# Kernel tuning notes

Hardware: AMD Instinct MI355X
Metric: run time of the kernel (lower is better)

Reference implementation:

```python
import jax, jax.numpy as jnp
import numpy as np

T, B = 128, 512
OBS_DIM = 512
HIDDEN = 512
ACTION_DIM = 18
LN_EPS = 1e-6  # flax LayerNorm default


def _layer_norm(x, scale, bias):
    m = jnp.mean(x, axis=-1, keepdims=True)
    v = jnp.var(x, axis=-1, keepdims=True)
    return (x - m) * jax.lax.rsqrt(v + LN_EPS) * scale + bias


def setup_inputs() -> dict:
    key = jax.random.key(0)
    ks = jax.random.split(key, 16)
    sc = lambda k, sh: jax.random.normal(k, sh, jnp.float32) * (1.0 / np.sqrt(sh[0]))
    d = {}
    d['hidden'] = jax.random.normal(ks[0], (B, HIDDEN), jnp.float32)
    d['obs'] = jax.random.normal(ks[1], (T, B, OBS_DIM), jnp.float32)
    d['dones'] = jax.random.randint(ks[2], (T, B), 0, 2).astype(bool)
    d['last_acts'] = jax.random.randint(ks[3], (T, B), 0, ACTION_DIM, dtype=jnp.int32)
    in0 = OBS_DIM + ACTION_DIM
    d['w0'] = sc(ks[4], (in0, HIDDEN)); d['b0'] = jnp.zeros((HIDDEN,), jnp.float32)
    d['ln0_s'] = jnp.ones((HIDDEN,), jnp.float32); d['ln0_b'] = jnp.zeros((HIDDEN,), jnp.float32)
    d['w1'] = sc(ks[5], (HIDDEN, HIDDEN)); d['b1'] = jnp.zeros((HIDDEN,), jnp.float32)
    d['ln1_s'] = jnp.ones((HIDDEN,), jnp.float32); d['ln1_b'] = jnp.zeros((HIDDEN,), jnp.float32)
    d['w_ir'] = sc(ks[6], (HIDDEN, HIDDEN)); d['b_ir'] = jnp.zeros((HIDDEN,), jnp.float32)
    d['w_iz'] = sc(ks[7], (HIDDEN, HIDDEN)); d['b_iz'] = jnp.zeros((HIDDEN,), jnp.float32)
    d['w_in'] = sc(ks[8], (HIDDEN, HIDDEN)); d['b_in'] = jnp.zeros((HIDDEN,), jnp.float32)
    d['w_hr'] = sc(ks[9], (HIDDEN, HIDDEN))
    d['w_hz'] = sc(ks[10], (HIDDEN, HIDDEN))
    d['w_hn'] = sc(ks[11], (HIDDEN, HIDDEN)); d['b_hn'] = jnp.zeros((HIDDEN,), jnp.float32)
    d['w_out'] = sc(ks[12], (HIDDEN, ACTION_DIM)); d['b_out'] = jnp.zeros((ACTION_DIM,), jnp.float32)
    return d


def reference(hidden, obs, dones, last_acts,
              w0, b0, ln0_s, ln0_b, w1, b1, ln1_s, ln1_b,
              w_ir, b_ir, w_iz, b_iz, w_in, b_in,
              w_hr, w_hz, w_hn, b_hn, w_out, b_out):
    # embed last actions and concat with obs: [T, B, obs_dim + action_dim]
    one_hot = jax.nn.one_hot(last_acts, ACTION_DIM, dtype=obs.dtype)
    x = jnp.concatenate([obs, one_hot], axis=-1)
    # MLP encoder: Dense -> LayerNorm -> relu, applied over all (T, B) at once
    x = jax.nn.relu(_layer_norm(x @ w0 + b0, ln0_s, ln0_b))
    x = jax.nn.relu(_layer_norm(x @ w1 + b1, ln1_s, ln1_b))

    # ScannedRNN: GRUCell with reset-to-zero carry on done, scanned over time
    def step(h, xs):
        xt, dt = xs  # xt: [B, H], dt: [B] bool
        h = jnp.where(dt[:, None], jnp.zeros_like(h), h)
        r = jax.nn.sigmoid(xt @ w_ir + b_ir + h @ w_hr)
        z = jax.nn.sigmoid(xt @ w_iz + b_iz + h @ w_hz)
        n = jnp.tanh(xt @ w_in + b_in + r * (h @ w_hn + b_hn))
        h_new = (1.0 - z) * n + z * h
        return h_new, h_new

    new_hidden, y = jax.lax.scan(step, hidden, (x, dones))
    q_vals = y @ w_out + b_out  # [T, B, action_dim]
    return new_hidden, q_vals
```

## Files before the change

### kernel.cpp

```cpp
#include <hip/hip_runtime.h>
#include <cstdint>
#include <cstddef>


#define TT 128
#define BBATCH 512
#define HH 512
#define MM 65536
#define AD 18
#define GSTEPS 8
#define FSTRIDE 32
#define READY_U32 1064960

typedef __attribute__((ext_vector_type(8))) short short8;
typedef __attribute__((ext_vector_type(4))) float float4v;
typedef __attribute__((ext_vector_type(4))) unsigned int uint4v;

__device__ __forceinline__ unsigned short f2bf(float f) {
  union { float f; unsigned int u; } v; v.f = f;
  unsigned int r = v.u + 0x7fffu + ((v.u >> 16) & 1u);
  return (unsigned short)(r >> 16);
}
__device__ __forceinline__ float bf2f(unsigned short h) {
  union { unsigned int u; float f; } v; v.u = ((unsigned int)h) << 16;
  return v.f;
}

__device__ __forceinline__ unsigned int load_u32_coh(const unsigned int* p) {
  unsigned int v;
  asm volatile("global_load_dword %0, %1, off sc0 sc1\n\ts_waitcnt vmcnt(0)"
               : "=v"(v) : "v"(p) : "memory");
  return v;
}
__device__ __forceinline__ void store_u32_coh(unsigned int* p, unsigned int v) {
  asm volatile("global_store_dword %0, %1, off sc0 sc1"
               :: "v"(p), "v"(v) : "memory");
}
__device__ __forceinline__ void store_u64_coh(void* p, unsigned long long v) {
  asm volatile("global_store_dwordx2 %0, %1, off sc0 sc1"
               :: "v"(p), "v"(v) : "memory");
}

typedef __attribute__((address_space(3))) unsigned int* lds_u32p;
typedef const __attribute__((address_space(1))) unsigned int* glb_u32p;
__device__ __forceinline__ void async16(void* lds, const void* g) {
  __builtin_amdgcn_global_load_lds(
      (glb_u32p)(unsigned long long)g,
      (lds_u32p)(unsigned int)(unsigned long long)lds, 16, 0, 0);
}


__global__ __launch_bounds__(256) void k_conv_obs(
    const float* __restrict__ src, unsigned short* __restrict__ dst,
    unsigned int* __restrict__ flag) {
  if (blockIdx.x == 0 && threadIdx.x == 0) *flag = 0u;
  int i = blockIdx.x * 256 + threadIdx.x;
  float4v v = ((const float4v*)src)[i];
  unsigned long long pk = (unsigned long long)f2bf(v[0])
      | ((unsigned long long)f2bf(v[1]) << 16)
      | ((unsigned long long)f2bf(v[2]) << 32)
      | ((unsigned long long)f2bf(v[3]) << 48);
  ((unsigned long long*)dst)[i] = pk;
}

__global__ __launch_bounds__(256) void k_prep_t(
    const float* __restrict__ w0, const float* __restrict__ w1,
    const float* __restrict__ wir, const float* __restrict__ wiz,
    const float* __restrict__ win,
    unsigned short* __restrict__ W0at, unsigned short* __restrict__ W1t,
    unsigned short* __restrict__ Wit) {
  int o = blockIdx.x * 256 + threadIdx.x;
  int n = o >> 9, k = o & 511;
  int z = blockIdx.y;
  const float* s = (z == 0) ? w0 : (z == 1) ? w1 : (z == 2) ? wir
                 : (z == 3) ? wiz : win;
  unsigned short b = f2bf(s[k * 512 + n]);
  if (z == 0) W0at[o] = b;
  else if (z == 1) W1t[o] = b;
  else Wit[(size_t)(z - 2) * 262144 + o] = b;
}

__global__ __launch_bounds__(256) void k_prep_whf(
    const float* __restrict__ whr, const float* __restrict__ whz,
    const float* __restrict__ whn, unsigned short* __restrict__ Whf) {
  int i = blockIdx.x * 256 + threadIdx.x;
  int k = i / 1536, n = i - k * 1536;
  const float* s = (n < 512) ? whr : (n < 1024) ? whz : whn;
  float v = s[k * 512 + (n & 511)];
  Whf[((size_t)(k >> 3) * 1536 + n) * 8 + (k & 7)] = f2bf(v);
}

__global__ __launch_bounds__(256) void k_prep_misc(
    const float* __restrict__ w0, const float* __restrict__ bir,
    const float* __restrict__ biz, const float* __restrict__ bin,
    const float* __restrict__ wout, const float* __restrict__ hidden,
    const int* __restrict__ dI,
    unsigned short* __restrict__ w0act, float* __restrict__ gib,
    unsigned short* __restrict__ WoutT, unsigned short* __restrict__ hbuf,
    unsigned int* __restrict__ flag) {
  int i = blockIdx.x * 256 + threadIdx.x;
  if (i < 9216) {
    int a = i >> 9, n = i & 511;
    w0act[i] = f2bf(w0[(512 + a) * 512 + n]);
  }
  if (i < 1536)
    gib[i] = (i < 512) ? bir[i] : (i < 1024) ? biz[i - 512] : bin[i - 1024];
  if (i < 32768) {
    int n = i >> 9, k = i & 511;
    WoutT[i] = f2bf(n < AD ? wout[k * AD + n] : 0.f);
  }
  if (i < 262144) hbuf[i] = f2bf(hidden[i]);
  if (i < 16384) { if (dI[i] & 0xFFFFFFFE) atomicOr(flag, 1u); }
}

__global__ __launch_bounds__(256) void k_zero(unsigned int* __restrict__ p) {
  int i = (blockIdx.x * 256 + threadIdx.x) * 4;
  if (i < READY_U32) *(uint4v*)(p + i) = (uint4v){0u, 0u, 0u, 0u};
}


template <int MODE>
__global__ __launch_bounds__(512, 1) void k_enc(
    const unsigned short* __restrict__ Ab,
    const unsigned short* __restrict__ Btb,
    unsigned short* __restrict__ Cb,
    const float* __restrict__ bias,
    const float* __restrict__ lnS, const float* __restrict__ lnB,
    const unsigned short* __restrict__ gW,
    const int* __restrict__ acts) {
  __shared__ unsigned short As[8192];
  __shared__ unsigned short Bs[32768];
  __shared__ float part[128][4][2];
  __shared__ float stats[128][2];

  const int tid = threadIdx.x, wave = tid >> 6, lane = tid & 63;
  const int quad = lane >> 4, l15 = lane & 15;
  const int wm = wave >> 2, wn = wave & 3;
  const int m0 = blockIdx.x * 128;
  const int g = (MODE == 2) ? blockIdx.y : 0;
  const unsigned short* Bt = Btb + (size_t)g * 262144;
  const float* bi = bias + g * 512;

  float4v acc[4][8];
#pragma unroll
  for (int a = 0; a < 4; ++a)
#pragma unroll
    for (int b = 0; b < 8; ++b) acc[a][b] = (float4v){0.f, 0.f, 0.f, 0.f};

  for (int k0 = 0; k0 < 512; k0 += 64) {
#pragma unroll
    for (int r = 0; r < 2; ++r) {
      int u = r * 512 + tid;
      int ch = u >> 7, mm = u & 127;
      async16(&As[(size_t)(r * 512 + wave * 64) * 8],
              Ab + (size_t)(m0 + mm) * 512 + k0 + ch * 8);
    }
#pragma unroll
    for (int r = 0; r < 8; ++r) {
      int u = r * 512 + tid;
      int ch = u >> 9, nn = u & 511;
      async16(&Bs[(size_t)(r * 512 + wave * 64) * 8],
              Bt + (size_t)nn * 512 + k0 + ch * 8);
    }
    __syncthreads();
#pragma unroll
    for (int kk = 0; kk < 2; ++kk) {
      short8 afr[4], bfr[8];
#pragma unroll
      for (int mi = 0; mi < 4; ++mi)
        afr[mi] = *(const short8*)
            &As[((kk * 4 + quad) * 128 + wm * 64 + mi * 16 + l15) * 8];
#pragma unroll
      for (int ni = 0; ni < 8; ++ni)
        bfr[ni] = *(const short8*)
            &Bs[((kk * 4 + quad) * 512 + wn * 128 + ni * 16 + l15) * 8];
#pragma unroll
      for (int mi = 0; mi < 4; ++mi)
#pragma unroll
        for (int ni = 0; ni < 8; ++ni)
          acc[mi][ni] = __builtin_amdgcn_mfma_f32_16x16x32_bf16(
              afr[mi], bfr[ni], acc[mi][ni], 0, 0, 0);
    }
    __syncthreads();
  }

  float bcol[8];
#pragma unroll
  for (int ni = 0; ni < 8; ++ni) bcol[ni] = bi[wn * 128 + ni * 16 + l15];
#pragma unroll
  for (int mi = 0; mi < 4; ++mi)
#pragma unroll
    for (int i = 0; i < 4; ++i) {
      int row = m0 + wm * 64 + mi * 16 + quad * 4 + i;
      int arow = (MODE == 0) ? acts[row] : 0;
#pragma unroll
      for (int ni = 0; ni < 8; ++ni) {
        float v = acc[mi][ni][i] + bcol[ni];
        if (MODE == 0) v += bf2f(gW[arow * 512 + wn * 128 + ni * 16 + l15]);
        acc[mi][ni][i] = v;
      }
    }

  if (MODE <= 1) {
#pragma unroll
    for (int mi = 0; mi < 4; ++mi)
#pragma unroll
      for (int i = 0; i < 4; ++i) {
        float s = 0.f, q = 0.f;
#pragma unroll
        for (int ni = 0; ni < 8; ++ni) {
          float v = acc[mi][ni][i];
          s += v; q += v * v;
        }
#pragma unroll
        for (int d = 1; d < 16; d <<= 1) {
          s += __shfl_xor(s, d, 64);
          q += __shfl_xor(q, d, 64);
        }
        if (l15 == 0) {
          int rowl = wm * 64 + mi * 16 + quad * 4 + i;
          part[rowl][wn][0] = s;
          part[rowl][wn][1] = q;
        }
      }
    __syncthreads();
    if (tid < 128) {
      float s = part[tid][0][0] + part[tid][1][0] + part[tid][2][0] + part[tid][3][0];
      float q = part[tid][0][1] + part[tid][1][1] + part[tid][2][1] + part[tid][3][1];
      float mean = s * (1.f / 512.f);
      float var = fmaxf(q * (1.f / 512.f) - mean * mean, 0.f);
      stats[tid][0] = mean;
      stats[tid][1] = rsqrtf(var + 1e-6f);
    }
    __syncthreads();
    float sc8[8], cb8[8];
#pragma unroll
    for (int ni = 0; ni < 8; ++ni) {
      int col = wn * 128 + ni * 16 + l15;
      sc8[ni] = lnS[col];
      cb8[ni] = lnB[col];
    }
#pragma unroll
    for (int mi = 0; mi < 4; ++mi)
#pragma unroll
      for (int i = 0; i < 4; ++i) {
        int rowl = wm * 64 + mi * 16 + quad * 4 + i;
        float mean = stats[rowl][0], rstd = stats[rowl][1];
        int row = m0 + rowl;
#pragma unroll
        for (int ni = 0; ni < 8; ++ni) {
          int col = wn * 128 + ni * 16 + l15;
          float v = fmaxf((acc[mi][ni][i] - mean) * rstd * sc8[ni] + cb8[ni], 0.f);
          Cb[(size_t)row * 512 + col] = f2bf(v);
        }
      }
  } else {
#pragma unroll
    for (int mi = 0; mi < 4; ++mi)
#pragma unroll
      for (int i = 0; i < 4; ++i) {
        int row = m0 + wm * 64 + mi * 16 + quad * 4 + i;
        int t = row >> 9, b = row & 511;
#pragma unroll
        for (int ni = 0; ni < 8; ++ni) {
          int c = wn * 128 + ni * 16 + l15;
          size_t dst = ((size_t)((b >> 6) * 32 + (c >> 4)) * 128 + t) * 3072
                     + (size_t)g * 1024 + (b & 63) * 16 + (c & 15);
          Cb[dst] = f2bf(acc[mi][ni][i]);
        }
      }
  }
}


__global__ __launch_bounds__(256, 1) void k_gru(
    const unsigned short* __restrict__ Whf, const unsigned short* __restrict__ gin,
    const float* __restrict__ bhn, const int* __restrict__ dI,
    const unsigned char* __restrict__ dB, const unsigned int* __restrict__ flag,
    const unsigned short* __restrict__ hbuf, unsigned short* __restrict__ ybuf,
    float* __restrict__ outh, unsigned int* __restrict__ ready) {
  __shared__ __align__(16) unsigned short gin_lds[2][GSTEPS * 3 * 64 * 16];
  __shared__ unsigned char d_lds[TT * 64];

  const int tid = threadIdx.x, wave = tid >> 6, lane = tid & 63;
  const int quad = lane >> 4, l15 = lane & 15;
  const int rt = blockIdx.x & 7;
  const int cc = blockIdx.x >> 3;
  const int r0b = rt * 64;
  const int rowb = wave * 16 + l15;
  const int row = r0b + rowb;
  const int c0 = cc * 16 + quad * 4;
  const int bytemode = (int)(*flag);
  const float4v bhn4 = *(const float4v*)(bhn + c0);

  const unsigned short* gsrc = gin + (size_t)(rt * 32 + cc) * 128 * 3072;

  auto stage_gin = [&](int buf, int t0) {
    const unsigned short* src = gsrc + (size_t)t0 * 3072;
#pragma unroll
    for (int r = 0; r < 12; ++r) {
      async16(&gin_lds[buf][(size_t)(r * 256 + wave * 64) * 8],
              src + (size_t)(r * 256 + tid) * 8);
    }
  };

  stage_gin(0, 0);
#pragma unroll
  for (int r = 0; r < 32; ++r) {
    int idx = r * 256 + tid;
    int t = idx >> 6, rr = idx & 63;
    int gidx = t * 512 + r0b + rr;
    d_lds[idx] = bytemode ? dB[gidx] : (unsigned char)(dI[gidx] != 0);
  }

  short8 bw[3][16];
#pragma unroll
  for (int kc = 0; kc < 16; ++kc)
#pragma unroll
    for (int g = 0; g < 3; ++g) {
      size_t u = (size_t)(kc * 4 + quad) * 1536 + (g * 512 + cc * 16 + l15);
      bw[g][kc] = *(const short8*)(Whf + u * 8);
    }

  float hprev[4];
  {
    unsigned long long w = *(const unsigned long long*)(hbuf + (size_t)row * 512 + c0);
#pragma unroll
    for (int i = 0; i < 4; ++i) hprev[i] = bf2f((unsigned short)(w >> (16 * i)));
  }

  __syncthreads();

  for (int t = 0; t < TT; ++t) {
    if (t > 0) {
      if (wave == 0) {
        const unsigned int* fp =
            ready + (((size_t)rt * 130 + t) * 32 + (lane & 31)) * FSTRIDE;
        unsigned int v;
        int guard = 0;
        do {
          v = load_u32_coh(fp);
        } while (__ballot(v == 0u) != 0ull && ++guard < (1 << 22));
      }
      __syncthreads();
      asm volatile("" ::: "memory");
    }

    const unsigned short* hsrc =
        (t == 0) ? hbuf : ybuf + (size_t)(t - 1) * 262144;
    const unsigned short* ap = hsrc + (size_t)row * 512 + quad * 8;
    short8 af[16];
#pragma unroll
    for (int kc = 0; kc < 16; ++kc) af[kc] = *(const short8*)(ap + kc * 32);

    const int dd = (int)d_lds[(t << 6) + rowb];
    if (dd) {
      const short8 z8 = {0, 0, 0, 0, 0, 0, 0, 0};
#pragma unroll
      for (int kc = 0; kc < 16; ++kc) af[kc] = z8;
    }

    if ((t & (GSTEPS - 1)) == 0 && t + GSTEPS < TT)
      stage_gin(((t >> 3) + 1) & 1, t + GSTEPS);

    const int sl = t & (GSTEPS - 1), bufc = (t >> 3) & 1;
    float gr[4], gz[4], gn[4];
    {
      const unsigned short* gl =
          &gin_lds[bufc][((size_t)(sl * 3) * 64 + rowb) * 16 + quad * 4];
      unsigned long long w0 = *(const unsigned long long*)(gl);
      unsigned long long w1 = *(const unsigned long long*)(gl + 1024);
      unsigned long long w2 = *(const unsigned long long*)(gl + 2048);
#pragma unroll
      for (int i = 0; i < 4; ++i) {
        gr[i] = bf2f((unsigned short)(w0 >> (16 * i)));
        gz[i] = bf2f((unsigned short)(w1 >> (16 * i)));
        gn[i] = bf2f((unsigned short)(w2 >> (16 * i)));
      }
    }

    float4v a0 = {0.f, 0.f, 0.f, 0.f}, a1 = a0, a2 = a0;
#pragma unroll
    for (int kc = 0; kc < 16; ++kc) {
      a0 = __builtin_amdgcn_mfma_f32_16x16x32_bf16(bw[0][kc], af[kc], a0, 0, 0, 0);
      a1 = __builtin_amdgcn_mfma_f32_16x16x32_bf16(bw[1][kc], af[kc], a1, 0, 0, 0);
      a2 = __builtin_amdgcn_mfma_f32_16x16x32_bf16(bw[2][kc], af[kc], a2, 0, 0, 0);
    }

    unsigned short* ydst = ybuf + (size_t)t * 262144;
    float hv[4];
#pragma unroll
    for (int i = 0; i < 4; ++i) {
      float hold = dd ? 0.f : hprev[i];
      float r = 1.f / (1.f + __expf(-(a0[i] + gr[i])));
      float z = 1.f / (1.f + __expf(-(a1[i] + gz[i])));
      float npre = gn[i] + r * (a2[i] + bhn4[i]);
      float n = 1.f - 2.f / (1.f + __expf(2.f * npre));
      hv[i] = (1.f - z) * n + z * hold;
      hprev[i] = hv[i];
    }
    {
      unsigned long long pk = (unsigned long long)f2bf(hv[0])
          | ((unsigned long long)f2bf(hv[1]) << 16)
          | ((unsigned long long)f2bf(hv[2]) << 32)
          | ((unsigned long long)f2bf(hv[3]) << 48);
      store_u64_coh(ydst + (size_t)row * 512 + c0, pk);
    }
    if (t == TT - 1) {
      float4v o = {hv[0], hv[1], hv[2], hv[3]};
      *(float4v*)(outh + (size_t)row * 512 + c0) = o;
    }

    __syncthreads();
    if (tid == 0)
      store_u32_coh(&ready[(((size_t)rt * 130 + t + 1) * 32 + cc) * FSTRIDE], 1u);
  }
}


__global__ __launch_bounds__(256) void k_qout(
    const unsigned short* __restrict__ Yb, const unsigned short* __restrict__ Wt,
    const float* __restrict__ bout, float* __restrict__ Q) {
  __shared__ unsigned short As[8192];
  __shared__ unsigned short Bs[4096];
  const int tid = threadIdx.x, wave = tid >> 6, lane = tid & 63;
  const int quad = lane >> 4, l15 = lane & 15;
  const int m0 = blockIdx.x * 128;

  float4v acc[2][4];
#pragma unroll
  for (int a = 0; a < 2; ++a)
#pragma unroll
    for (int b = 0; b < 4; ++b) acc[a][b] = (float4v){0.f, 0.f, 0.f, 0.f};

  for (int k0 = 0; k0 < 512; k0 += 64) {
#pragma unroll
    for (int r = 0; r < 4; ++r) {
      int u = r * 256 + wave * 64 + lane;
      int ch = u >> 7, mm = u & 127;
      async16(&As[(size_t)(r * 256 + wave * 64) * 8],
              Yb + (size_t)(m0 + mm) * 512 + k0 + ch * 8);
    }
#pragma unroll
    for (int r = 0; r < 2; ++r) {
      int u = r * 256 + wave * 64 + lane;
      int ch = u >> 6, nn = u & 63;
      async16(&Bs[(size_t)(r * 256 + wave * 64) * 8],
              Wt + (size_t)nn * 512 + k0 + ch * 8);
    }
    __syncthreads();
#pragma unroll
    for (int kk = 0; kk < 2; ++kk) {
      short8 afr[2], bfr[4];
#pragma unroll
      for (int mi = 0; mi < 2; ++mi)
        afr[mi] = *(const short8*)
            &As[((kk * 4 + quad) * 128 + wave * 32 + mi * 16 + l15) * 8];
#pragma unroll
      for (int ni = 0; ni < 4; ++ni)
        bfr[ni] = *(const short8*)
            &Bs[((kk * 4 + quad) * 64 + ni * 16 + l15) * 8];
#pragma unroll
      for (int mi = 0; mi < 2; ++mi)
#pragma unroll
        for (int ni = 0; ni < 4; ++ni)
          acc[mi][ni] = __builtin_amdgcn_mfma_f32_16x16x32_bf16(
              afr[mi], bfr[ni], acc[mi][ni], 0, 0, 0);
    }
    __syncthreads();
  }
#pragma unroll
  for (int mi = 0; mi < 2; ++mi)
#pragma unroll
    for (int ni = 0; ni < 4; ++ni)
#pragma unroll
      for (int i = 0; i < 4; ++i) {
        int row = m0 + wave * 32 + mi * 16 + quad * 4 + i;
        int colq = ni * 16 + l15;
        if (colq < AD) Q[(size_t)row * AD + colq] = acc[mi][ni][i] + bout[colq];
      }
}


extern "C" void kernel_launch(void* const* d_in, const int* in_sizes, int n_in,
                              void* d_out, int out_size, void* d_ws,
                              size_t ws_size, hipStream_t stream) {
  const float* hidden = (const float*)d_in[0];
  const float* obs = (const float*)d_in[1];
  const void* dones = d_in[2];
  const int* acts = (const int*)d_in[3];
  const float* w0 = (const float*)d_in[4];
  const float* b0 = (const float*)d_in[5];
  const float* ln0s = (const float*)d_in[6];
  const float* ln0b = (const float*)d_in[7];
  const float* w1 = (const float*)d_in[8];
  const float* b1 = (const float*)d_in[9];
  const float* ln1s = (const float*)d_in[10];
  const float* ln1b = (const float*)d_in[11];
  const float* wir = (const float*)d_in[12];
  const float* bir = (const float*)d_in[13];
  const float* wiz = (const float*)d_in[14];
  const float* biz = (const float*)d_in[15];
  const float* win = (const float*)d_in[16];
  const float* bin = (const float*)d_in[17];
  const float* whr = (const float*)d_in[18];
  const float* whz = (const float*)d_in[19];
  const float* whn = (const float*)d_in[20];
  const float* bhn = (const float*)d_in[21];
  const float* wout = (const float*)d_in[22];
  const float* bout = (const float*)d_in[23];

  char* ws = (char*)d_ws;
  unsigned short* bufA = (unsigned short*)(ws);
  unsigned short* bufB = (unsigned short*)(ws + 67108864ULL);
  unsigned short* gin = (unsigned short*)(ws + 134217728ULL);
  char* D = ws + 134217728ULL + 201326592ULL;
  unsigned short* W0at = (unsigned short*)(D);
  unsigned short* W1t = (unsigned short*)(D + 524288);
  unsigned short* Wit = (unsigned short*)(D + 1048576);
  unsigned short* Whf = (unsigned short*)(D + 2621440);
  unsigned short* WoutT = (unsigned short*)(D + 4194304);
  unsigned short* w0act = (unsigned short*)(D + 4259840);
  float* gib = (float*)(D + 4292608);
  unsigned short* hbuf = (unsigned short*)(D + 4300800);
  unsigned int* flag = (unsigned int*)(D + 4825088);
  unsigned int* ready = (unsigned int*)ws;

  (void)in_sizes; (void)n_in; (void)out_size; (void)ws_size;

  k_conv_obs<<<32768, 256, 0, stream>>>(obs, bufA, flag);
  k_prep_t<<<dim3(1024, 5), 256, 0, stream>>>(w0, w1, wir, wiz, win, W0at, W1t, Wit);
  k_prep_whf<<<3072, 256, 0, stream>>>(whr, whz, whn, Whf);
  k_prep_misc<<<1024, 256, 0, stream>>>(w0, bir, biz, bin, wout, hidden,
                                        (const int*)dones, w0act, gib, WoutT,
                                        hbuf, flag);
  k_enc<0><<<512, 512, 0, stream>>>(bufA, W0at, bufB, b0, ln0s, ln0b, w0act, acts);
  k_enc<1><<<512, 512, 0, stream>>>(bufB, W1t, bufA, b1, ln1s, ln1b, nullptr, nullptr);
  k_enc<2><<<dim3(512, 3), 512, 0, stream>>>(bufA, Wit, gin, gib, nullptr, nullptr,
                                             nullptr, nullptr);
  k_zero<<<1041, 256, 0, stream>>>(ready);
  k_gru<<<256, 256, 0, stream>>>(Whf, gin, bhn, (const int*)dones,
                                 (const unsigned char*)dones, flag, hbuf, bufB,
                                 (float*)d_out, ready);
  k_qout<<<512, 256, 0, stream>>>(bufB, WoutT, bout, (float*)d_out + 262144);
}
```

Baseline: 1.230 ms.

## Fuse obs bf16 conversion into first encoder GEMM and merge prep kernels

Removes the separate pass that converts obs from fp32 to bf16. The first encoder GEMM now loads fp32 obs tiles asynchronously into a larger LDS buffer and converts them to bf16 when building MFMA fragments. The three weight-prep kernels are merged into one launch, and the dones flag check becomes a single-block ballot reduction instead of atomics. This saves a 128MB read plus a 64MB write pass and several launches, at the cost of more LDS, double the A-tile traffic and extra conversion ALU work inside the GEMM.

```diff
diff --git a/kernel.cpp b/kernel.cpp
--- a/kernel.cpp
+++ b/kernel.cpp
@@ -50,67 +50,60 @@
 }
 
 
-__global__ __launch_bounds__(256) void k_conv_obs(
-    const float* __restrict__ src, unsigned short* __restrict__ dst,
-    unsigned int* __restrict__ flag) {
-  if (blockIdx.x == 0 && threadIdx.x == 0) *flag = 0u;
-  int i = blockIdx.x * 256 + threadIdx.x;
-  float4v v = ((const float4v*)src)[i];
-  unsigned long long pk = (unsigned long long)f2bf(v[0])
-      | ((unsigned long long)f2bf(v[1]) << 16)
-      | ((unsigned long long)f2bf(v[2]) << 32)
-      | ((unsigned long long)f2bf(v[3]) << 48);
-  ((unsigned long long*)dst)[i] = pk;
-}
-
-__global__ __launch_bounds__(256) void k_prep_t(
+__global__ __launch_bounds__(256) void k_prep(
     const float* __restrict__ w0, const float* __restrict__ w1,
     const float* __restrict__ wir, const float* __restrict__ wiz,
     const float* __restrict__ win,
+    const float* __restrict__ whr, const float* __restrict__ whz,
+    const float* __restrict__ whn,
+    const float* __restrict__ bir, const float* __restrict__ biz,
+    const float* __restrict__ bin, const float* __restrict__ wout,
+    const float* __restrict__ hidden, const int* __restrict__ dI,
     unsigned short* __restrict__ W0at, unsigned short* __restrict__ W1t,
-    unsigned short* __restrict__ Wit) {
-  int o = blockIdx.x * 256 + threadIdx.x;
-  int n = o >> 9, k = o & 511;
-  int z = blockIdx.y;
-  const float* s = (z == 0) ? w0 : (z == 1) ? w1 : (z == 2) ? wir
-                 : (z == 3) ? wiz : win;
-  unsigned short b = f2bf(s[k * 512 + n]);
-  if (z == 0) W0at[o] = b;
-  else if (z == 1) W1t[o] = b;
-  else Wit[(size_t)(z - 2) * 262144 + o] = b;
-}
-
-__global__ __launch_bounds__(256) void k_prep_whf(
-    const float* __restrict__ whr, const float* __restrict__ whz,
-    const float* __restrict__ whn, unsigned short* __restrict__ Whf) {
-  int i = blockIdx.x * 256 + threadIdx.x;
-  int k = i / 1536, n = i - k * 1536;
-  const float* s = (n < 512) ? whr : (n < 1024) ? whz : whn;
-  float v = s[k * 512 + (n & 511)];
-  Whf[((size_t)(k >> 3) * 1536 + n) * 8 + (k & 7)] = f2bf(v);
-}
-
-__global__ __launch_bounds__(256) void k_prep_misc(
-    const float* __restrict__ w0, const float* __restrict__ bir,
-    const float* __restrict__ biz, const float* __restrict__ bin,
-    const float* __restrict__ wout, const float* __restrict__ hidden,
-    const int* __restrict__ dI,
+    unsigned short* __restrict__ Wit, unsigned short* __restrict__ Whf,
     unsigned short* __restrict__ w0act, float* __restrict__ gib,
     unsigned short* __restrict__ WoutT, unsigned short* __restrict__ hbuf,
     unsigned int* __restrict__ flag) {
   int i = blockIdx.x * 256 + threadIdx.x;
-  if (i < 9216) {
-    int a = i >> 9, n = i & 511;
-    w0act[i] = f2bf(w0[(512 + a) * 512 + n]);
-  }
-  if (i < 1536)
-    gib[i] = (i < 512) ? bir[i] : (i < 1024) ? biz[i - 512] : bin[i - 1024];
-  if (i < 32768) {
-    int n = i >> 9, k = i & 511;
-    WoutT[i] = f2bf(n < AD ? wout[k * AD + n] : 0.f);
-  }
-  if (i < 262144) hbuf[i] = f2bf(hidden[i]);
-  if (i < 16384) { if (dI[i] & 0xFFFFFFFE) atomicOr(flag, 1u); }
+  if (i < 1310720) {
+    int o = i & 262143, z = i >> 18;
+    int n = o >> 9, k = o & 511;
+    const float* s = (z == 0) ? w0 : (z == 1) ? w1 : (z == 2) ? wir
+                   : (z == 3) ? wiz : win;
+    unsigned short b = f2bf(s[k * 512 + n]);
+    if (z == 0) W0at[o] = b;
+    else if (z == 1) W1t[o] = b;
+    else Wit[(size_t)(z - 2) * 262144 + o] = b;
+  } else if (i < 2097152) {
+    int j = i - 1310720;
+    int k = j / 1536, n = j - k * 1536;
+    const float* s = (n < 512) ? whr : (n < 1024) ? whz : whn;
+    Whf[((size_t)(k >> 3) * 1536 + n) * 8 + (k & 7)] = f2bf(s[k * 512 + (n & 511)]);
+  } else {
+    int j = i - 2097152;
+    if (j < 9216) {
+      int a = j >> 9, n = j & 511;
+      w0act[j] = f2bf(w0[(512 + a) * 512 + n]);
+    }
+    if (j < 1536)
+      gib[j] = (j < 512) ? bir[j] : (j < 1024) ? biz[j - 512] : bin[j - 1024];
+    if (j < 32768) {
+      int n = j >> 9, k = j & 511;
+      WoutT[j] = f2bf(n < AD ? wout[k * AD + n] : 0.f);
+    }
+    hbuf[j] = f2bf(hidden[j]);
+  }
+  if (blockIdx.x == 9215) {
+    __shared__ int wany[4];
+    int t = threadIdx.x;
+    int any = 0;
+#pragma unroll 8
+    for (int v = 0; v < 64; ++v) any |= dI[t * 64 + v] & 0xFFFFFFFE;
+    unsigned long long b = __ballot(any != 0);
+    if ((t & 63) == 0) wany[t >> 6] = (b != 0ull) ? 1 : 0;
+    __syncthreads();
+    if (t == 0) *flag = (unsigned int)(wany[0] | wany[1] | wany[2] | wany[3]);
+  }
 }
 
 __global__ __launch_bounds__(256) void k_zero(unsigned int* __restrict__ p) {
@@ -128,10 +121,12 @@
     const float* __restrict__ lnS, const float* __restrict__ lnB,
     const unsigned short* __restrict__ gW,
     const int* __restrict__ acts) {
-  __shared__ unsigned short As[8192];
+  __shared__ __align__(16) unsigned char AsRaw[MODE == 0 ? 32768 : 16384];
   __shared__ unsigned short Bs[32768];
   __shared__ float part[128][4][2];
   __shared__ float stats[128][2];
+  float* Asf = (float*)AsRaw;
+  unsigned short* Ash = (unsigned short*)AsRaw;
 
   const int tid = threadIdx.x, wave = tid >> 6, lane = tid & 63;
   const int quad = lane >> 4, l15 = lane & 15;
@@ -148,12 +143,23 @@
     for (int b = 0; b < 8; ++b) acc[a][b] = (float4v){0.f, 0.f, 0.f, 0.f};
 
   for (int k0 = 0; k0 < 512; k0 += 64) {
-#pragma unroll
-    for (int r = 0; r < 2; ++r) {
-      int u = r * 512 + tid;
-      int ch = u >> 7, mm = u & 127;
-      async16(&As[(size_t)(r * 512 + wave * 64) * 8],
-              Ab + (size_t)(m0 + mm) * 512 + k0 + ch * 8);
+    if constexpr (MODE == 0) {
+      const float* Af = (const float*)Ab;
+#pragma unroll
+      for (int r = 0; r < 4; ++r) {
+        int u = r * 512 + tid;
+        int ch = u >> 8, rem = u & 255, mm = rem >> 1, half = rem & 1;
+        async16(&Asf[(size_t)(r * 512 + wave * 64) * 4],
+                Af + (size_t)(m0 + mm) * 512 + k0 + ch * 8 + half * 4);
+      }
+    } else {
+#pragma unroll
+      for (int r = 0; r < 2; ++r) {
+        int u = r * 512 + tid;
+        int ch = u >> 7, mm = u & 127;
+        async16(&Ash[(size_t)(r * 512 + wave * 64) * 8],
+                Ab + (size_t)(m0 + mm) * 512 + k0 + ch * 8);
+      }
     }
 #pragma unroll
     for (int r = 0; r < 8; ++r) {
@@ -167,9 +173,24 @@
     for (int kk = 0; kk < 2; ++kk) {
       short8 afr[4], bfr[8];
 #pragma unroll
-      for (int mi = 0; mi < 4; ++mi)
-        afr[mi] = *(const short8*)
-            &As[((kk * 4 + quad) * 128 + wm * 64 + mi * 16 + l15) * 8];
+      for (int mi = 0; mi < 4; ++mi) {
+        int mrow = wm * 64 + mi * 16 + l15;
+        if constexpr (MODE == 0) {
+          const float* ap = &Asf[(size_t)((kk * 4 + quad) * 128 + mrow) * 8];
+          float4v lo = *(const float4v*)ap;
+          float4v hi = *(const float4v*)(ap + 4);
+          short8 f;
+#pragma unroll
+          for (int j = 0; j < 4; ++j) {
+            f[j] = (short)f2bf(lo[j]);
+            f[j + 4] = (short)f2bf(hi[j]);
+          }
+          afr[mi] = f;
+        } else {
+          afr[mi] = *(const short8*)
+              &Ash[(size_t)((kk * 4 + quad) * 128 + mrow) * 8];
+        }
+      }
 #pragma unroll
       for (int ni = 0; ni < 8; ++ni)
         bfr[ni] = *(const short8*)
@@ -528,16 +549,16 @@
 
   (void)in_sizes; (void)n_in; (void)out_size; (void)ws_size;
 
-  k_conv_obs<<<32768, 256, 0, stream>>>(obs, bufA, flag);
-  k_prep_t<<<dim3(1024, 5), 256, 0, stream>>>(w0, w1, wir, wiz, win, W0at, W1t, Wit);
-  k_prep_whf<<<3072, 256, 0, stream>>>(whr, whz, whn, Whf);
-  k_prep_misc<<<1024, 256, 0, stream>>>(w0, bir, biz, bin, wout, hidden,
-                                        (const int*)dones, w0act, gib, WoutT,
-                                        hbuf, flag);
-  k_enc<0><<<512, 512, 0, stream>>>(bufA, W0at, bufB, b0, ln0s, ln0b, w0act, acts);
-  k_enc<1><<<512, 512, 0, stream>>>(bufB, W1t, bufA, b1, ln1s, ln1b, nullptr, nullptr);
-  k_enc<2><<<dim3(512, 3), 512, 0, stream>>>(bufA, Wit, gin, gib, nullptr, nullptr,
-                                             nullptr, nullptr);
+  k_prep<<<9216, 256, 0, stream>>>(w0, w1, wir, wiz, win, whr, whz, whn,
+                                   bir, biz, bin, wout, hidden,
+                                   (const int*)dones, W0at, W1t, Wit, Whf,
+                                   w0act, gib, WoutT, hbuf, flag);
+  k_enc<0><<<512, 512, 0, stream>>>((const unsigned short*)obs, W0at, bufB,
+                                    b0, ln0s, ln0b, w0act, acts);
+  k_enc<1><<<512, 512, 0, stream>>>(bufB, W1t, bufA, b1, ln1s, ln1b,
+                                    nullptr, nullptr);
+  k_enc<2><<<dim3(512, 3), 512, 0, stream>>>(bufA, Wit, gin, gib, nullptr,
+                                             nullptr, nullptr, nullptr);
   k_zero<<<1041, 256, 0, stream>>>(ready);
   k_gru<<<256, 256, 0, stream>>>(Whf, gin, bhn, (const int*)dones,
                                  (const unsigned char*)dones, flag, hbuf, bufB,
```

New measurement: 1.221 ms. About the same (-0.8%).
